# Optimization experiments

Hardware: AMD Instinct MI355X
Metric: run time of the kernel (lower is better)

The kernel has to match this reference:

```python
import jax, jax.numpy as jnp
import numpy as np
from jax import lax

VOCAB = 1000
TMAX = 1001  # max_episode_length + 1
L = 2048
H_GRU = 256


def setup_inputs() -> dict:
    key = jax.random.key(0)
    ks = jax.random.split(key, 40)
    g = lambda i, shape, s: jax.random.normal(ks[i], shape, dtype=jnp.float32) * s
    inp = {
        "x": jax.random.normal(ks[0], (1, 3, 124, 124), dtype=jnp.float32),
        "curr_instr": jax.random.randint(ks[1], (1, L), 0, VOCAB),
        "prev_instr": jax.random.randint(ks[2], (1, L), 0, VOCAB),
        "next_instr": jax.random.randint(ks[3], (1, L), 0, VOCAB),
        "tx": jax.random.randint(ks[4], (1,), 0, TMAX),
        "hx": jnp.zeros((1, 768), jnp.float32),
        "cx": jnp.zeros((1, 768), jnp.float32),
        # conv stack
        "conv1_w": g(5, (128, 3, 8, 8), 0.05), "conv1_b": jnp.zeros((128,), jnp.float32),
        "conv2_w": g(6, (64, 128, 4, 4), 0.03), "conv2_b": jnp.zeros((64,), jnp.float32),
        "conv3_w": g(7, (64, 64, 4, 4), 0.03), "conv3_b": jnp.zeros((64,), jnp.float32),
        # embeddings
        "emb": g(8, (VOCAB, 32), 0.1),
        "time_emb": g(9, (TMAX, 32), 0.1),
        # GRU (torch nn.GRU layout: 3*H rows for r,z,n)
        "gru_w_ih": g(10, (3 * H_GRU, 32), 0.1), "gru_w_hh": g(11, (3 * H_GRU, H_GRU), 0.06),
        "gru_b_ih": jnp.zeros((3 * H_GRU,), jnp.float32), "gru_b_hh": jnp.zeros((3 * H_GRU,), jnp.float32),
        # attention linear 256 -> 64
        "attn_w": g(12, (64, H_GRU), 0.06), "attn_b": jnp.zeros((64,), jnp.float32),
        # image-fusion linear 64*6*6 -> 256
        "lin_w": g(13, (256, 64 * 6 * 6), 0.02), "lin_b": jnp.zeros((256,), jnp.float32),
        # LSTMCell 768 -> 768 (torch layout: 4*H rows for i,f,g,o)
        "lstm_w_ih": g(14, (4 * 768, 768), 0.03), "lstm_w_hh": g(15, (4 * 768, 768), 0.03),
        "lstm_b_ih": jnp.zeros((4 * 768,), jnp.float32), "lstm_b_hh": jnp.zeros((4 * 768,), jnp.float32),
        # heads over [hx, time_emb] = 768 + 32 = 800
        "critic_w": g(16, (1, 800), 0.03), "critic_b": jnp.zeros((1,), jnp.float32),
        "actor_w": g(17, (4, 800), 0.01), "actor_b": jnp.zeros((4,), jnp.float32),
    }
    return inp


def _conv(x, w, b, s):
    return lax.conv_general_dilated(x, w, (s, s), "VALID") + b[None, :, None, None]


def reference(x, curr_instr, prev_instr, next_instr, tx, hx, cx,
              conv1_w, conv1_b, conv2_w, conv2_b, conv3_w, conv3_b,
              emb, time_emb, gru_w_ih, gru_w_hh, gru_b_ih, gru_b_hh,
              attn_w, attn_b, lin_w, lin_b,
              lstm_w_ih, lstm_w_hh, lstm_b_ih, lstm_b_hh,
              critic_w, critic_b, actor_w, actor_b):
    # image tower: [1,3,124,124] -> [1,64,6,6]
    h1 = jax.nn.relu(_conv(x, conv1_w, conv1_b, 4))
    h2 = jax.nn.relu(_conv(h1, conv2_w, conv2_b, 2))
    x_image_rep = jax.nn.relu(_conv(h2, conv3_w, conv3_b, 2))

    # three instruction sequences, encoded by a shared GRU (vmapped scan)
    tokens = jnp.stack([curr_instr[0], prev_instr[0], next_instr[0]])  # [3, L]

    def gru_encode(tok):
        xs = emb[tok]                               # [L, 32]
        gi_all = xs @ gru_w_ih.T + gru_b_ih         # precompute input gates [L, 3H]
        def step(h, gi):
            gh = h @ gru_w_hh.T + gru_b_hh
            i_r, i_z, i_n = jnp.split(gi, 3)
            h_r, h_z, h_n = jnp.split(gh, 3)
            r = jax.nn.sigmoid(i_r + h_r)
            z = jax.nn.sigmoid(i_z + h_z)
            n = jnp.tanh(i_n + r * h_n)
            return (1.0 - z) * n + z * h, None
        h, _ = lax.scan(step, jnp.zeros((H_GRU,), xs.dtype), gi_all)
        return h

    h3 = jax.vmap(gru_encode)(tokens)               # [3, 256]
    attn = jax.nn.sigmoid(h3 @ attn_w.T + attn_b)   # [3, 64]

    # BUG-FAITHFUL: original forward uses cached_computation['curr_x_attention']
    # for all three branches, so the three fused features are identical.
    curr_attn = attn[0][None, :, None, None]        # [1,64,1,1]
    fused = (x_image_rep * curr_attn).reshape(1, -1)  # [1, 2304]
    feat = jax.nn.relu(fused @ lin_w.T + lin_b)     # [1, 256]
    xcat = jnp.concatenate([feat, feat, feat], axis=1)  # [1, 768]

    # LSTMCell
    gates = xcat @ lstm_w_ih.T + lstm_b_ih + hx @ lstm_w_hh.T + lstm_b_hh  # [1, 3072]
    gi, gf, gg, go = jnp.split(gates, 4, axis=1)
    cx_new = jax.nn.sigmoid(gf) * cx + jax.nn.sigmoid(gi) * jnp.tanh(gg)
    hx_new = jax.nn.sigmoid(go) * jnp.tanh(cx_new)

    t = time_emb[tx].reshape(-1, 32)                # [1, 32]
    z = jnp.concatenate([hx_new, t], axis=1)        # [1, 800]
    critic = z @ critic_w.T + critic_b              # [1, 1]
    actor = z @ actor_w.T + actor_b                 # [1, 4]
    return critic, actor, hx_new, cx_new
```

## Files before the change

kernel.cpp:

```cpp
#include <hip/hip_runtime.h>
#include <hip/hip_bf16.h>
#include <stdint.h>


typedef _Float16 half8 __attribute__((ext_vector_type(8)));
typedef _Float16 half2v __attribute__((ext_vector_type(2)));
typedef float f32x4 __attribute__((ext_vector_type(4)));

__device__ __forceinline__ float sigm(float x) { return 1.0f / (1.0f + __expf(-x)); }
__device__ __forceinline__ float tanh_f(float x) { return 2.0f / (1.0f + __expf(-2.0f * x)) - 1.0f; }

__global__ void k_pack(const float* __restrict__ whh, uint32_t* __restrict__ wf16p) {
    int i = blockIdx.x * 256 + threadIdx.x;
    if (i >= 98304) return;
    half2v p = {(_Float16)whh[2 * i], (_Float16)whh[2 * i + 1]};
    wf16p[i] = __builtin_bit_cast(uint32_t, p);
}

__global__ void k_conv1(const float* __restrict__ x, const float* __restrict__ w,
                        const float* __restrict__ b, float* __restrict__ h1) {
    int idx = blockIdx.x * 256 + threadIdx.x;
    if (idx >= 128 * 30 * 30) return;
    int ox = idx % 30, oy = (idx / 30) % 30, oc = idx / 900;
    const float* wr = w + oc * 192;
    float acc = b[oc];
    for (int c = 0; c < 3; ++c)
        for (int ky = 0; ky < 8; ++ky) {
            const float* xr = x + (c * 124 + oy * 4 + ky) * 124 + ox * 4;
            const float* wk = wr + (c * 8 + ky) * 8;
#pragma unroll
            for (int kx = 0; kx < 8; ++kx) acc = fmaf(xr[kx], wk[kx], acc);
        }
    h1[idx] = fmaxf(acc, 0.0f);
}

__global__ void k_conv2(const float* __restrict__ h1, const float* __restrict__ w,
                        const float* __restrict__ b, float* __restrict__ h2) {
    int idx = blockIdx.x * 256 + threadIdx.x;
    if (idx >= 64 * 14 * 14) return;
    int ox = idx % 14, oy = (idx / 14) % 14, oc = idx / 196;
    float acc = b[oc];
    const float* wr = w + oc * 128 * 16;
    for (int c = 0; c < 128; ++c) {
#pragma unroll
        for (int ky = 0; ky < 4; ++ky) {
            const float* hr = h1 + (c * 30 + oy * 2 + ky) * 30 + ox * 2;
            const float* wk = wr + (c * 4 + ky) * 4;
#pragma unroll
            for (int kx = 0; kx < 4; ++kx) acc = fmaf(hr[kx], wk[kx], acc);
        }
    }
    h2[idx] = fmaxf(acc, 0.0f);
}

__global__ void k_conv3(const float* __restrict__ h2, const float* __restrict__ w,
                        const float* __restrict__ b, float* __restrict__ x3) {
    int idx = blockIdx.x * 256 + threadIdx.x;
    if (idx >= 64 * 6 * 6) return;
    int ox = idx % 6, oy = (idx / 6) % 6, oc = idx / 36;
    float acc = b[oc];
    const float* wr = w + oc * 64 * 16;
    for (int c = 0; c < 64; ++c) {
#pragma unroll
        for (int ky = 0; ky < 4; ++ky) {
            const float* hr = h2 + (c * 14 + oy * 2 + ky) * 14 + ox * 2;
            const float* wk = wr + (c * 4 + ky) * 4;
#pragma unroll
            for (int kx = 0; kx < 4; ++kx) acc = fmaf(hr[kx], wk[kx], acc);
        }
    }
    x3[idx] = fmaxf(acc, 0.0f);
}

__global__ void k_gi(const int* __restrict__ curr, const float* __restrict__ emb,
                     const float* __restrict__ wih, const float* __restrict__ bih,
                     float* __restrict__ gi) {
    int idx = blockIdx.x * 256 + threadIdx.x;
    int j = idx % 768, t = idx / 768;
    int tok = curr[t];
    const float4* e = (const float4*)(emb + tok * 32);
    const float4* wr = (const float4*)(wih + j * 32);
    float acc = bih[j];
#pragma unroll
    for (int k = 0; k < 8; ++k) {
        float4 ev = e[k], wv = wr[k];
        acc = fmaf(ev.x, wv.x, acc);
        acc = fmaf(ev.y, wv.y, acc);
        acc = fmaf(ev.z, wv.z, acc);
        acc = fmaf(ev.w, wv.w, acc);
    }
    gi[idx] = acc;
}

#define FOR8(X, nt) X(nt, 0) X(nt, 1) X(nt, 2) X(nt, 3) X(nt, 4) X(nt, 5) X(nt, 6) X(nt, 7)
#define FOR6(Y) Y(0) Y(1) Y(2) Y(3) Y(4) Y(5)

#define DECLB(nt, kt) uint4 b##nt##_##kt;
#define DECLBROW(nt) FOR8(DECLB, nt)
#define LOADB(nt, kt) b##nt##_##kt = wp4[nt * 512 + kt * 4 + quad];
#define LOADBROW(nt) FOR8(LOADB, nt)
#define TIEB(nt, kt) \
    asm volatile("" : "+v"(b##nt##_##kt.x), "+v"(b##nt##_##kt.y), "+v"(b##nt##_##kt.z), "+v"(b##nt##_##kt.w));
#define TIEBROW(nt) FOR8(TIEB, nt)
#define DECLBIAS(nt) const float bias##nt = bhh[wbase + nt * 16 + n16];
#define DECLACC(nt) f32x4 acc##nt;
#define ZEROACC(nt) acc##nt = (f32x4)(0.0f);
#define MF(nt, kt) \
    acc##nt = __builtin_amdgcn_mfma_f32_16x16x32_f16(a##kt, __builtin_bit_cast(half8, b##nt##_##kt), acc##nt, 0, 0, 0);
#define MFK(kt) MF(0, kt) MF(1, kt) MF(2, kt) MF(3, kt) MF(4, kt) MF(5, kt)
#define LOADA(kt) half8 a##kt = __builtin_bit_cast(half8, abase[kt * 4 + quad]);
#define EPI(nt) \
    if (lane < 16) gh[wbase + nt * 16 + lane] = acc##nt.x + acc##nt.y * 0.0009765625f + bias##nt;

__global__ __attribute__((amdgpu_flat_work_group_size(512, 512), amdgpu_waves_per_eu(2, 2)))
void k_gru_scan(const float* __restrict__ gi, const uint32_t* __restrict__ wf16p,
                const float* __restrict__ bhh, const float* __restrict__ attn_w,
                const float* __restrict__ attn_b, float* __restrict__ attn0) {
    __shared__ __align__(16) _Float16 hhi[256];
    __shared__ __align__(16) _Float16 hlo[256];
    __shared__ float gh[768];
    const int tid = threadIdx.x;
    const int lane = tid & 63;
    const int wv = tid >> 6;
    const int n16 = lane & 15;
    const int quad = lane >> 4;
    const int wbase = wv * 96;

    FOR6(DECLBROW)
    {
        const uint4* wp4 = (const uint4*)(wf16p + (size_t)(wbase + n16) * 128);
        FOR6(LOADBROW)
    }
    FOR6(TIEBROW)
    FOR6(DECLBIAS)
    FOR6(DECLACC)

    float h_own = 0.0f;
    if (tid < 256) {
        hhi[tid] = (_Float16)0.0f;
        hlo[tid] = (_Float16)0.0f;
    }
    float gv0 = 0.f, gv1 = 0.f, gv2 = 0.f;
    if (tid < 256) {
        gv0 = gi[tid];
        gv1 = gi[256 + tid];
        gv2 = gi[512 + tid];
    }
    __syncthreads();

    const uint4* abase = (n16 == 1) ? (const uint4*)hlo : (const uint4*)hhi;

#pragma clang loop unroll(disable)
    for (int step = 0; step < 2048; ++step) {
        float gn0 = 0.f, gn1 = 0.f, gn2 = 0.f;
        if (step < 2047 && tid < 256) {
            const float* gp = gi + (size_t)(step + 1) * 768 + tid;
            gn0 = gp[0]; gn1 = gp[256]; gn2 = gp[512];
        }

        FOR6(ZEROACC)
        LOADA(0) LOADA(1)
        MFK(0)
        LOADA(2)
        MFK(1)
        LOADA(3)
        MFK(2)
        LOADA(4)
        MFK(3)
        LOADA(5)
        MFK(4)
        LOADA(6)
        MFK(5)
        LOADA(7)
        MFK(6)
        MFK(7)

        FOR6(EPI)
        __syncthreads();

        if (tid < 256) {
            float r = sigm(gv0 + gh[tid]);
            float z = sigm(gv1 + gh[256 + tid]);
            float n = tanh_f(fmaf(r, gh[512 + tid], gv2));
            h_own = fmaf(z, h_own - n, n);
            _Float16 hi16 = (_Float16)h_own;
            hhi[tid] = hi16;
            hlo[tid] = (_Float16)((h_own - (float)hi16) * 1024.0f);
        }
        gv0 = gn0; gv1 = gn1; gv2 = gn2;
        __syncthreads();
    }

    if (tid < 64) {
        const float* ar = attn_w + tid * 256;
        float acc = attn_b[tid];
        for (int k = 0; k < 256; ++k) {
            float hk = (float)hhi[k] + (float)hlo[k] * 0.0009765625f;
            acc = fmaf(ar[k], hk, acc);
        }
        attn0[tid] = sigm(acc);
    }
}

__global__ void k_feat(const float* __restrict__ x3, const float* __restrict__ attn0,
                       const float* __restrict__ lw, const float* __restrict__ lb,
                       float* __restrict__ feat) {
    __shared__ __align__(16) float fused[2304];
    int t = threadIdx.x;
    for (int i = t; i < 2304; i += 64) fused[i] = x3[i] * attn0[i / 36];
    __syncthreads();
    int row = blockIdx.x * 64 + t;
    const float4* wvv = (const float4*)(lw + (size_t)row * 2304);
    float acc = lb[row];
    for (int i = 0; i < 576; ++i) {
        float4 v = wvv[i];
        const float* f = fused + i * 4;
        acc = fmaf(v.x, f[0], acc);
        acc = fmaf(v.y, f[1], acc);
        acc = fmaf(v.z, f[2], acc);
        acc = fmaf(v.w, f[3], acc);
    }
    feat[row] = fmaxf(acc, 0.0f);
}

__global__ void k_lstm_gates(const float* __restrict__ wih, const float* __restrict__ whh,
                             const float* __restrict__ bih, const float* __restrict__ bhh,
                             const float* __restrict__ hx, const float* __restrict__ feat,
                             float* __restrict__ gates) {
    int wid = threadIdx.x >> 6, lane = threadIdx.x & 63;
    int row = blockIdx.x * 4 + wid;
    const float* wi = wih + (size_t)row * 768;
    const float* wh = whh + (size_t)row * 768;
    float acc = 0.0f;
#pragma unroll
    for (int i = 0; i < 12; ++i) {
        int k = lane + i * 64;
        acc = fmaf(wi[k], feat[k & 255], acc);
        acc = fmaf(wh[k], hx[k], acc);
    }
#pragma unroll
    for (int s = 32; s; s >>= 1) acc += __shfl_down(acc, s, 64);
    if (lane == 0) gates[row] = acc + bih[row] + bhh[row];
}

__global__ void k_lstm_cell(const float* __restrict__ gates, const float* __restrict__ cx,
                            float* __restrict__ out, float* __restrict__ hxf) {
    int i = threadIdx.x;
    float g_i = gates[i], g_f = gates[768 + i], g_g = gates[1536 + i], g_o = gates[2304 + i];
    float c = cx[i];
    float cn = sigm(g_f) * c + sigm(g_i) * tanh_f(g_g);
    float hn = sigm(g_o) * tanh_f(cn);
    out[5 + i] = hn;
    out[5 + 768 + i] = cn;
    hxf[i] = hn;
}

__global__ void k_heads(const float* __restrict__ hxf, const float* __restrict__ temb,
                        const int* __restrict__ tx, const float* __restrict__ cw,
                        const float* __restrict__ cb, const float* __restrict__ aw,
                        const float* __restrict__ ab, float* __restrict__ out) {
    __shared__ float z[800];
    int t = threadIdx.x;
    for (int i = t; i < 768; i += 320) z[i] = hxf[i];
    if (t < 32) z[768 + t] = temb[tx[0] * 32 + t];
    __syncthreads();
    int w = t >> 6, lane = t & 63;
    const float* row = (w == 0) ? cw : (aw + (size_t)(w - 1) * 800);
    float acc = 0.0f;
    for (int k = lane; k < 800; k += 64) acc = fmaf(row[k], z[k], acc);
#pragma unroll
    for (int s = 32; s; s >>= 1) acc += __shfl_down(acc, s, 64);
    if (lane == 0) {
        float b = (w == 0) ? cb[0] : ab[w - 1];
        out[w] = acc + b;
    }
}

extern "C" void kernel_launch(void* const* d_in, const int* in_sizes, int n_in,
                              void* d_out, int out_size, void* d_ws, size_t ws_size,
                              hipStream_t stream) {
    const float* x = (const float*)d_in[0];
    const int* curr = (const int*)d_in[1];
    const int* tx = (const int*)d_in[4];
    const float* hx = (const float*)d_in[5];
    const float* cx = (const float*)d_in[6];
    const float* c1w = (const float*)d_in[7];
    const float* c1b = (const float*)d_in[8];
    const float* c2w = (const float*)d_in[9];
    const float* c2b = (const float*)d_in[10];
    const float* c3w = (const float*)d_in[11];
    const float* c3b = (const float*)d_in[12];
    const float* emb = (const float*)d_in[13];
    const float* temb = (const float*)d_in[14];
    const float* gwih = (const float*)d_in[15];
    const float* gwhh = (const float*)d_in[16];
    const float* gbih = (const float*)d_in[17];
    const float* gbhh = (const float*)d_in[18];
    const float* attw = (const float*)d_in[19];
    const float* attb = (const float*)d_in[20];
    const float* linw = (const float*)d_in[21];
    const float* linb = (const float*)d_in[22];
    const float* lwih = (const float*)d_in[23];
    const float* lwhh = (const float*)d_in[24];
    const float* lbih = (const float*)d_in[25];
    const float* lbhh = (const float*)d_in[26];
    const float* cw = (const float*)d_in[27];
    const float* cb = (const float*)d_in[28];
    const float* aw = (const float*)d_in[29];
    const float* ab = (const float*)d_in[30];
    float* out = (float*)d_out;

    char* ws = (char*)d_ws;
    float* gi = (float*)(ws + 0);
    float* h1 = (float*)(ws + 6291456);
    float* h2 = (float*)(ws + 6752256);
    float* x3 = (float*)(ws + 6802432);
    float* attn0 = (float*)(ws + 6811648);
    float* feat = (float*)(ws + 6811904);
    float* gates = (float*)(ws + 6812928);
    float* hxf = (float*)(ws + 6825216);
    uint32_t* wf16p = (uint32_t*)(ws + 6828288);

    k_pack<<<384, 256, 0, stream>>>(gwhh, wf16p);
    k_gi<<<6144, 256, 0, stream>>>(curr, emb, gwih, gbih, gi);
    k_conv1<<<450, 256, 0, stream>>>(x, c1w, c1b, h1);
    k_conv2<<<49, 256, 0, stream>>>(h1, c2w, c2b, h2);
    k_conv3<<<9, 256, 0, stream>>>(h2, c3w, c3b, x3);
    k_gru_scan<<<1, 512, 0, stream>>>(gi, wf16p, gbhh, attw, attb, attn0);
    k_feat<<<4, 64, 0, stream>>>(x3, attn0, linw, linb, feat);
    k_lstm_gates<<<768, 256, 0, stream>>>(lwih, lwhh, lbih, lbhh, hx, feat, gates);
    k_lstm_cell<<<1, 768, 0, stream>>>(gates, cx, out, hxf);
    k_heads<<<1, 320, 0, stream>>>(hxf, temb, tx, cw, cb, aw, ab, out);
}
```

Measured before the change: 2.578 ms.

## Split GRU scan across 12 waves and interleave hi/lo hidden state buffer

The serial GRU scan now runs 768 threads (12 waves), each wave owning 4 output tiles of 16 rows instead of 6, which shortens the per-step MFMA chain per wave. The hi and lo fp16 halves of the hidden state are interleaved into one shared buffer in 32-element chunks, so the A-operand loads for both halves come from one base with a fixed offset. This adds more waves that take part in each step's barriers, which may raise per-step sync cost in exchange for less MFMA latency per wave.

```diff
diff --git a/kernel.cpp b/kernel.cpp
--- a/kernel.cpp
+++ b/kernel.cpp
@@ -93,7 +93,7 @@
 }
 
 #define FOR8(X, nt) X(nt, 0) X(nt, 1) X(nt, 2) X(nt, 3) X(nt, 4) X(nt, 5) X(nt, 6) X(nt, 7)
-#define FOR6(Y) Y(0) Y(1) Y(2) Y(3) Y(4) Y(5)
+#define FOR4(Y) Y(0) Y(1) Y(2) Y(3)
 
 #define DECLB(nt, kt) uint4 b##nt##_##kt;
 #define DECLBROW(nt) FOR8(DECLB, nt)
@@ -107,39 +107,35 @@
 #define ZEROACC(nt) acc##nt = (f32x4)(0.0f);
 #define MF(nt, kt) \
     acc##nt = __builtin_amdgcn_mfma_f32_16x16x32_f16(a##kt, __builtin_bit_cast(half8, b##nt##_##kt), acc##nt, 0, 0, 0);
-#define MFK(kt) MF(0, kt) MF(1, kt) MF(2, kt) MF(3, kt) MF(4, kt) MF(5, kt)
-#define LOADA(kt) half8 a##kt = __builtin_bit_cast(half8, abase[kt * 4 + quad]);
+#define MFK(kt) MF(0, kt) MF(1, kt) MF(2, kt) MF(3, kt)
+#define LOADA(kt) half8 a##kt = __builtin_bit_cast(half8, abase[kt * 8 + quad]);
 #define EPI(nt) \
     if (lane < 16) gh[wbase + nt * 16 + lane] = acc##nt.x + acc##nt.y * 0.0009765625f + bias##nt;
 
-__global__ __attribute__((amdgpu_flat_work_group_size(512, 512), amdgpu_waves_per_eu(2, 2)))
+__global__ __attribute__((amdgpu_flat_work_group_size(768, 768), amdgpu_waves_per_eu(3, 3)))
 void k_gru_scan(const float* __restrict__ gi, const uint32_t* __restrict__ wf16p,
                 const float* __restrict__ bhh, const float* __restrict__ attn_w,
                 const float* __restrict__ attn_b, float* __restrict__ attn0) {
-    __shared__ __align__(16) _Float16 hhi[256];
-    __shared__ __align__(16) _Float16 hlo[256];
+    __shared__ __align__(16) _Float16 hbuf[512];
     __shared__ float gh[768];
     const int tid = threadIdx.x;
     const int lane = tid & 63;
     const int wv = tid >> 6;
     const int n16 = lane & 15;
     const int quad = lane >> 4;
-    const int wbase = wv * 96;
-
-    FOR6(DECLBROW)
+    const int wbase = wv * 64;
+
+    FOR4(DECLBROW)
     {
         const uint4* wp4 = (const uint4*)(wf16p + (size_t)(wbase + n16) * 128);
-        FOR6(LOADBROW)
-    }
-    FOR6(TIEBROW)
-    FOR6(DECLBIAS)
-    FOR6(DECLACC)
+        FOR4(LOADBROW)
+    }
+    FOR4(TIEBROW)
+    FOR4(DECLBIAS)
+    FOR4(DECLACC)
 
     float h_own = 0.0f;
-    if (tid < 256) {
-        hhi[tid] = (_Float16)0.0f;
-        hlo[tid] = (_Float16)0.0f;
-    }
+    if (tid < 512) hbuf[tid] = (_Float16)0.0f;
     float gv0 = 0.f, gv1 = 0.f, gv2 = 0.f;
     if (tid < 256) {
         gv0 = gi[tid];
@@ -148,7 +144,8 @@
     }
     __syncthreads();
 
-    const uint4* abase = (n16 == 1) ? (const uint4*)hlo : (const uint4*)hhi;
+    const uint4* abase = (const uint4*)hbuf + ((n16 == 1) ? 4 : 0);
+    const int hwc = (tid >> 5) * 64 + (tid & 31);
 
 #pragma clang loop unroll(disable)
     for (int step = 0; step < 2048; ++step) {
@@ -158,7 +155,7 @@
             gn0 = gp[0]; gn1 = gp[256]; gn2 = gp[512];
         }
 
-        FOR6(ZEROACC)
+        FOR4(ZEROACC)
         LOADA(0) LOADA(1)
         MFK(0)
         LOADA(2)
@@ -175,7 +172,7 @@
         MFK(6)
         MFK(7)
 
-        FOR6(EPI)
+        FOR4(EPI)
         __syncthreads();
 
         if (tid < 256) {
@@ -184,8 +181,8 @@
             float n = tanh_f(fmaf(r, gh[512 + tid], gv2));
             h_own = fmaf(z, h_own - n, n);
             _Float16 hi16 = (_Float16)h_own;
-            hhi[tid] = hi16;
-            hlo[tid] = (_Float16)((h_own - (float)hi16) * 1024.0f);
+            hbuf[hwc] = hi16;
+            hbuf[hwc + 32] = (_Float16)((h_own - (float)hi16) * 1024.0f);
         }
         gv0 = gn0; gv1 = gn1; gv2 = gn2;
         __syncthreads();
@@ -195,7 +192,8 @@
         const float* ar = attn_w + tid * 256;
         float acc = attn_b[tid];
         for (int k = 0; k < 256; ++k) {
-            float hk = (float)hhi[k] + (float)hlo[k] * 0.0009765625f;
+            int c = k >> 5, i = k & 31;
+            float hk = (float)hbuf[c * 64 + i] + (float)hbuf[c * 64 + 32 + i] * 0.0009765625f;
             acc = fmaf(ar[k], hk, acc);
         }
         attn0[tid] = sigm(acc);
@@ -326,7 +324,7 @@
     k_conv1<<<450, 256, 0, stream>>>(x, c1w, c1b, h1);
     k_conv2<<<49, 256, 0, stream>>>(h1, c2w, c2b, h2);
     k_conv3<<<9, 256, 0, stream>>>(h2, c3w, c3b, x3);
-    k_gru_scan<<<1, 512, 0, stream>>>(gi, wf16p, gbhh, attw, attb, attn0);
+    k_gru_scan<<<1, 768, 0, stream>>>(gi, wf16p, gbhh, attw, attb, attn0);
     k_feat<<<4, 64, 0, stream>>>(x3, attn0, linw, linb, feat);
     k_lstm_gates<<<768, 256, 0, stream>>>(lwih, lwhh, lbih, lbhh, hx, feat, gates);
     k_lstm_cell<<<1, 768, 0, stream>>>(gates, cx, out, hxf);
```

After: 2.715 ms. 1.05x slower.
